# Kernel tuning notes

Hardware: AMD Instinct MI355X
Metric: run time of the kernel (lower is better)

Reference implementation:

```python
import jax, jax.numpy as jnp
import numpy as np
from jax import lax

B, S, D, T = 128, 512, 512, 64
OUT = 3


def setup_inputs() -> dict:
    key = jax.random.key(0)
    ks = jax.random.split(key, 16)
    sd = 0.05
    return {
        "e_all": jax.random.normal(ks[0], (B, S, D), jnp.float32),
        "e_last": jax.random.normal(ks[1], (1, B, D), jnp.float32),
        "target": jax.random.normal(ks[2], (B, T, OUT), jnp.float32),
        # attention params
        "Wa": jax.random.normal(ks[3], (D, D), jnp.float32) * sd,
        "ba": jnp.zeros((D,), jnp.float32),
        "Ua": jax.random.normal(ks[4], (D, D), jnp.float32) * sd,
        "bu": jnp.zeros((D,), jnp.float32),
        "Va_w": jax.random.normal(ks[5], (1, D), jnp.float32) * sd,
        "Va_b": jnp.zeros((1,), jnp.float32),
        # GRU params (PyTorch layout: [3D, in], gates order r,z,n)
        "W_ih": jax.random.normal(ks[6], (3 * D, D + OUT), jnp.float32) * sd,
        "b_ih": jnp.zeros((3 * D,), jnp.float32),
        "W_hh": jax.random.normal(ks[7], (3 * D, D), jnp.float32) * sd,
        "b_hh": jnp.zeros((3 * D,), jnp.float32),
        # output projection
        "W_out": jax.random.normal(ks[8], (OUT, D), jnp.float32) * sd,
        "b_out": jnp.zeros((OUT,), jnp.float32),
    }


def reference(e_all, e_last, target, Wa, ba, Ua, bu, Va_w, Va_b,
              W_ih, b_ih, W_hh, b_hh, W_out, b_out):
    # Precompute Ua(keys): keys are fixed across timesteps (same math as per-step).
    Uk = jnp.einsum('bsd,ed->bse', e_all, Ua) + bu        # [B,S,D]
    va = Va_w[0]                                          # [D]

    def step(h, x):
        # h: [B,D] decoder hidden; x: [B,3] decoder input (dropout is eval/identity)
        q = h @ Wa.T + ba                                  # [B,D]
        scores = jnp.einsum('bsd,d->bs', jnp.tanh(q[:, None, :] + Uk), va) + Va_b[0]
        w = jax.nn.softmax(scores, axis=-1)                # [B,S]
        ctx = jnp.einsum('bs,bsd->bd', w, e_all)           # [B,D]
        gin = jnp.concatenate([ctx, x], axis=-1)           # [B,D+3]  (attn first)
        gi = gin @ W_ih.T + b_ih                           # [B,3D]
        gh = h @ W_hh.T + b_hh                             # [B,3D]
        i_r, i_z, i_n = jnp.split(gi, 3, axis=-1)
        h_r, h_z, h_n = jnp.split(gh, 3, axis=-1)
        r = jax.nn.sigmoid(i_r + h_r)
        z = jax.nn.sigmoid(i_z + h_z)
        n = jnp.tanh(i_n + r * h_n)
        h_new = (1.0 - z) * n + z * h                      # [B,D]
        out = h_new @ W_out.T + b_out                      # [B,3]
        return h_new, (out, w)

    # teacher forcing: step 0 sees zeros, step i sees target[:, i-1]
    xs = jnp.concatenate([jnp.zeros((1, B, OUT), e_all.dtype),
                          jnp.swapaxes(target[:, :T - 1, :], 0, 1)], axis=0)  # [T,B,3]
    hT, (outs, attns) = lax.scan(step, e_last[0], xs)
    d_outputs = jnp.swapaxes(outs, 0, 1)     # [B,T,3]
    cross_attn = jnp.swapaxes(attns, 0, 1)   # [B,T,S]
    return d_outputs, hT[None], cross_attn
```

## Files before the change

kernel.cpp:

```cpp
#include <hip/hip_runtime.h>
#include <cstdint>

constexpr int BB = 128;
constexpr int SS = 512;
constexpr int DD = 512;
constexpr int TT = 64;
constexpr int OO = 3;

constexpr float C2LE = 2.8853900817779268f;

typedef __attribute__((ext_vector_type(8))) short bf16x8;
typedef __attribute__((ext_vector_type(4))) float f32x4;

__device__ __forceinline__ float tanh_fast(float x) {
  float e = __expf(2.0f * x);
  return 1.0f - 2.0f / (e + 1.0f);
}
__device__ __forceinline__ float sigmoid_fast(float x) {
  return 1.0f / (1.0f + __expf(-x));
}
__device__ __forceinline__ unsigned short f2bf(float f) {
  uint32_t u = __float_as_uint(f);
  uint32_t r = (u + 0x7FFFu + ((u >> 16) & 1u)) >> 16;
  return (unsigned short)r;
}
__device__ __forceinline__ float bf2f(unsigned short h) {
  return __uint_as_float((uint32_t)h << 16);
}
__device__ __forceinline__ float2 bfx2(uint32_t u) {
  float2 r;
  r.x = __uint_as_float(u << 16);
  r.y = __uint_as_float(u & 0xFFFF0000u);
  return r;
}
__device__ __forceinline__ float fexp2(float x) {
#if __has_builtin(__builtin_amdgcn_exp2f)
  return __builtin_amdgcn_exp2f(x);
#else
  return exp2f(x);
#endif
}
__device__ __forceinline__ float frcp(float x) {
#if __has_builtin(__builtin_amdgcn_rcpf)
  return __builtin_amdgcn_rcpf(x);
#else
  return 1.0f / x;
#endif
}

__global__ __launch_bounds__(256) void gemm_uk_mfma(
    const unsigned short* __restrict__ A, const unsigned short* __restrict__ Bw,
    const float* __restrict__ bias, unsigned short* __restrict__ Uk) {
  __shared__ unsigned short Asb[128 * 40];
  __shared__ unsigned short Bsb[128 * 40];
  const int tid = threadIdx.x;
  const int m0 = blockIdx.y * 128, n0 = blockIdx.x * 128;
  const int w = tid >> 6, l = tid & 63;
  const int wr = w >> 1, wc = w & 1;
  const int lm = l & 15, kg = l >> 4;

  f32x4 acc[4][4] = {};

  for (int kc = 0; kc < 512; kc += 32) {
    uint4 av[2], bv[2];
#pragma unroll
    for (int p = 0; p < 2; ++p) {
      int u = tid + p * 256;
      int r = u >> 2, ko = (u & 3) * 8;
      av[p] = *(const uint4*)(A + (size_t)(m0 + r) * 512 + kc + ko);
      bv[p] = *(const uint4*)(Bw + (size_t)(n0 + r) * 512 + kc + ko);
    }
    __syncthreads();
#pragma unroll
    for (int p = 0; p < 2; ++p) {
      int u = tid + p * 256;
      int r = u >> 2, ko = (u & 3) * 8;
      *(uint4*)&Asb[r * 40 + ko] = av[p];
      *(uint4*)&Bsb[r * 40 + ko] = bv[p];
    }
    __syncthreads();
    bf16x8 af[4], bfr[4];
#pragma unroll
    for (int i = 0; i < 4; ++i) {
      af[i]  = *(const bf16x8*)&Asb[(wr * 64 + i * 16 + lm) * 40 + kg * 8];
      bfr[i] = *(const bf16x8*)&Bsb[(wc * 64 + i * 16 + lm) * 40 + kg * 8];
    }
#pragma unroll
    for (int i = 0; i < 4; ++i)
#pragma unroll
      for (int j = 0; j < 4; ++j)
        acc[i][j] = __builtin_amdgcn_mfma_f32_16x16x32_bf16(af[i], bfr[j],
                                                            acc[i][j], 0, 0, 0);
  }

  const int row_base = m0 + wr * 64;
  const int col_base = n0 + wc * 64;
#pragma unroll
  for (int j = 0; j < 4; ++j) {
    const int col = col_base + j * 16 + lm;
    const float bu = bias[col];
#pragma unroll
    for (int i = 0; i < 4; ++i) {
      const int r0 = row_base + i * 16 + kg * 4;
#pragma unroll
      for (int rr = 0; rr < 4; ++rr)
        Uk[(size_t)(r0 + rr) * 512 + col] = f2bf(C2LE * (acc[i][j][rr] + bu));
    }
  }
}

__global__ __launch_bounds__(256) void conv_bf(const float* __restrict__ in,
                                               unsigned short* __restrict__ outp) {
  size_t idx = ((size_t)blockIdx.x * 256 + threadIdx.x) * 8;
  const float4* p = (const float4*)(in + idx);
  float4 a = p[0], b = p[1];
  uint4 r;
  r.x = f2bf(a.x) | ((uint32_t)f2bf(a.y) << 16);
  r.y = f2bf(a.z) | ((uint32_t)f2bf(a.w) << 16);
  r.z = f2bf(b.x) | ((uint32_t)f2bf(b.y) << 16);
  r.w = f2bf(b.z) | ((uint32_t)f2bf(b.w) << 16);
  *(uint4*)(outp + idx) = r;
}

__global__ void prep_wq2(const float* __restrict__ Wa,
                         unsigned short* __restrict__ Wq2) {
  int idx = blockIdx.x * 256 + threadIdx.x;
  Wq2[idx] = f2bf(C2LE * Wa[idx]);
}

__global__ void prep_wih3(const float* __restrict__ W_ih,
                          unsigned short* __restrict__ Wih3) {
  int idx = blockIdx.x * 256 + threadIdx.x;
  int rp = idx >> 9, k = idx & 511;
  int dgrp = rp / 48, rem = rp % 48;
  int g = rem >> 4, dl = rem & 15;
  int src = g * 512 + dgrp * 16 + dl;
  Wih3[idx] = f2bf(W_ih[(size_t)src * (DD + OO) + k]);
}

__global__ void prep_whh3(const float* __restrict__ Whh,
                          unsigned short* __restrict__ Whh3) {
  int idx = blockIdx.x * 256 + threadIdx.x;
  int rp = idx >> 9, k = idx & 511;
  int dgrp = rp / 48, rem = rp % 48;
  int g = rem >> 4, dl = rem & 15;
  int src = g * 512 + dgrp * 16 + dl;
  Whh3[idx] = f2bf(Whh[(size_t)src * DD + k]);
}

__global__ void prep_bq(const float* __restrict__ ba, float* __restrict__ bq) {
  int j = blockIdx.x * 256 + threadIdx.x;
  bq[j] = C2LE * ba[j];
}

__global__ void init_h(const float* __restrict__ e_last,
                       float* __restrict__ out_hT,
                       unsigned short* __restrict__ h2g) {
  int idx = blockIdx.x * 256 + threadIdx.x;
  int b = idx >> 9, d = idx & 511;
  float v = e_last[idx];
  out_hT[idx] = v;
  unsigned short hi = f2bf(v);
  h2g[(size_t)b * 1024 + d] = hi;
  h2g[(size_t)b * 1024 + 512 + d] = f2bf(v - bf2f(hi));
}

__global__ __launch_bounds__(1024) void qgemm_out(
    const unsigned short* __restrict__ h2g, const unsigned short* __restrict__ Wq2,
    const float* __restrict__ bq, float* __restrict__ q2g,
    const float* __restrict__ out_hT, const float* __restrict__ W_out,
    const float* __restrict__ b_out, float* __restrict__ out_d, int t) {
  const int blk = blockIdx.x, tid = threadIdx.x;
  __shared__ unsigned short As[128 * 136];
  __shared__ unsigned short Bs[32 * 136];
  if (blk < 16) {
    const int w = tid >> 6, l = tid & 63, lm = l & 15, kg = l >> 4;
    const int n0 = blk * 32;
    const int mi = w >> 1, jt = w & 1;
    f32x4 acc = {};
    for (int kc = 0; kc < 1024; kc += 128) {
#pragma unroll
      for (int p = 0; p < 2; ++p) {
        int u = tid + p * 1024;
        int r = u >> 4, ko = (u & 15) * 8;
        *(uint4*)&As[r * 136 + ko] =
            *(const uint4*)&h2g[(size_t)r * 1024 + kc + ko];
      }
      if (tid < 512) {
        int r = tid >> 4, ko = (tid & 15) * 8;
        *(uint4*)&Bs[r * 136 + ko] =
            *(const uint4*)&Wq2[(size_t)(n0 + r) * 512 + (kc & 511) + ko];
      }
      __syncthreads();
#pragma unroll
      for (int ks = 0; ks < 4; ++ks) {
        bf16x8 af = *(const bf16x8*)&As[(mi * 16 + lm) * 136 + ks * 32 + kg * 8];
        bf16x8 bf_ = *(const bf16x8*)&Bs[(jt * 16 + lm) * 136 + ks * 32 + kg * 8];
        acc = __builtin_amdgcn_mfma_f32_16x16x32_bf16(af, bf_, acc, 0, 0, 0);
      }
      __syncthreads();
    }
    const int col = n0 + jt * 16 + lm;
    const float bias = bq[col];
#pragma unroll
    for (int rr = 0; rr < 4; ++rr) {
      const int b = mi * 16 + kg * 4 + rr;
      q2g[(size_t)b * 512 + col] = acc[rr] + bias;
    }
  } else if (t > 0) {
    const int b = tid >> 3, g8 = tid & 7;
    const float* hp = out_hT + (size_t)b * DD + g8 * 64;
#pragma unroll
    for (int o = 0; o < OO; ++o) {
      const float* wrow = W_out + (size_t)o * DD + g8 * 64;
      float acc = 0.f;
#pragma unroll 8
      for (int i = 0; i < 64; ++i) acc += hp[i] * wrow[i];
      acc += __shfl_down(acc, 4, 8);
      acc += __shfl_down(acc, 2, 8);
      acc += __shfl_down(acc, 1, 8);
      if (g8 == 0) out_d[((size_t)b * TT + (t - 1)) * OO + o] = acc + b_out[o];
    }
  }
}

__global__ __launch_bounds__(256) void attn_scores(
    const unsigned short* __restrict__ Uk2, const float* __restrict__ q2g,
    const float* __restrict__ va, float* __restrict__ scores) {
  const int b = blockIdx.y;
  const int s0 = blockIdx.x * 64;
  __shared__ float4 shq[DD / 4];
  __shared__ float4 shva[DD / 4];
  const int tid = threadIdx.x;
  if (tid < DD / 4) {
    shq[tid] = ((const float4*)(q2g + (size_t)b * DD))[tid];
    shva[tid] = ((const float4*)va)[tid];
  }
  __syncthreads();
  const int g = tid >> 4, l = tid & 15;
#pragma unroll
  for (int i = 0; i < 4; ++i) {
    const int s = s0 + 16 * i + g;
    const uint4* row = (const uint4*)(Uk2 + ((size_t)b * SS + s) * DD);
    float acc = 0.f;
#pragma unroll
    for (int jj = 0; jj < 4; ++jj) {
      const int slot = l + 16 * jj;
      uint4 u = row[slot];
      float4 q0 = shq[slot * 2], q1 = shq[slot * 2 + 1];
      float4 v0 = shva[slot * 2], v1 = shva[slot * 2 + 1];
      float2 e0 = bfx2(u.x), e1 = bfx2(u.y), e2 = bfx2(u.z), e3 = bfx2(u.w);
      acc += v0.x * frcp(1.f + fexp2(q0.x + e0.x));
      acc += v0.y * frcp(1.f + fexp2(q0.y + e0.y));
      acc += v0.z * frcp(1.f + fexp2(q0.z + e1.x));
      acc += v0.w * frcp(1.f + fexp2(q0.w + e1.y));
      acc += v1.x * frcp(1.f + fexp2(q1.x + e2.x));
      acc += v1.y * frcp(1.f + fexp2(q1.y + e2.y));
      acc += v1.z * frcp(1.f + fexp2(q1.z + e3.x));
      acc += v1.w * frcp(1.f + fexp2(q1.w + e3.y));
    }
#pragma unroll
    for (int off = 8; off; off >>= 1) acc += __shfl_down(acc, off, 16);
    if (l == 0) scores[(size_t)b * SS + s] = -2.f * acc;
  }
}

__global__ __launch_bounds__(256) void attn_ctx(
    const unsigned short* __restrict__ e_bf, const float* __restrict__ scores,
    float* __restrict__ ctx, float* __restrict__ attn_out, int t) {
  const int b = blockIdx.y, dc = blockIdx.x;
  __shared__ float w[SS];
  __shared__ float red[8];
  __shared__ float part[16][132];
  const int tid = threadIdx.x;

  float v0 = scores[(size_t)b * SS + tid];
  float v1 = scores[(size_t)b * SS + 256 + tid];
  float m = fmaxf(v0, v1);
#pragma unroll
  for (int off = 32; off; off >>= 1) m = fmaxf(m, __shfl_xor(m, off));
  if ((tid & 63) == 0) red[tid >> 6] = m;
  __syncthreads();
  m = fmaxf(fmaxf(red[0], red[1]), fmaxf(red[2], red[3]));
  float e0 = __expf(v0 - m), e1 = __expf(v1 - m);
  float ss = e0 + e1;
#pragma unroll
  for (int off = 32; off; off >>= 1) ss += __shfl_xor(ss, off);
  __syncthreads();
  if ((tid & 63) == 0) red[tid >> 6] = ss;
  __syncthreads();
  const float inv = 1.f / (red[0] + red[1] + red[2] + red[3]);
  float w0 = e0 * inv, w1 = e1 * inv;
  w[tid] = w0;
  w[tid + 256] = w1;
  if (dc == 0) {
    float* ao = attn_out + ((size_t)b * TT + t) * SS;
    ao[tid] = w0;
    ao[tid + 256] = w1;
  }
  __syncthreads();

  {
    const int sl = tid & 15, sg = tid >> 4;
    const unsigned short* eb = e_bf + (size_t)b * SS * DD + dc * 128 + sl * 8;
    float a0 = 0.f, a1 = 0.f, a2 = 0.f, a3 = 0.f;
    float a4 = 0.f, a5 = 0.f, a6 = 0.f, a7 = 0.f;
    for (int s = sg * 32; s < sg * 32 + 32; ++s) {
      uint4 u = *(const uint4*)(eb + (size_t)s * DD);
      float ws = w[s];
      float2 p0 = bfx2(u.x), p1 = bfx2(u.y), p2 = bfx2(u.z), p3 = bfx2(u.w);
      a0 += ws * p0.x; a1 += ws * p0.y;
      a2 += ws * p1.x; a3 += ws * p1.y;
      a4 += ws * p2.x; a5 += ws * p2.y;
      a6 += ws * p3.x; a7 += ws * p3.y;
    }
    float* pr = &part[sg][sl * 8];
    pr[0] = a0; pr[1] = a1; pr[2] = a2; pr[3] = a3;
    pr[4] = a4; pr[5] = a5; pr[6] = a6; pr[7] = a7;
  }
  __syncthreads();
  if (tid < 128) {
    const int sl = tid >> 3, c = tid & 7;
    float r = 0.f;
#pragma unroll
    for (int sg = 0; sg < 16; ++sg) r += part[sg][sl * 8 + c];
    ctx[(size_t)b * DD + dc * 128 + sl * 8 + c] = r;
  }
}

__global__ __launch_bounds__(1024) void gru_fused(
    const float* __restrict__ ctx, unsigned short* __restrict__ h2g,
    const unsigned short* __restrict__ Wih3, const unsigned short* __restrict__ Whh3,
    float* __restrict__ out_hT, const float* __restrict__ target,
    const float* __restrict__ W_ih, const float* __restrict__ b_ih,
    const float* __restrict__ b_hh, int t) {
  const int blk = blockIdx.x, tid = threadIdx.x;
  const int w = tid >> 6, l = tid & 63, lm = l & 15, kg = l >> 4;
  const int mh = blk >> 5, dgrp = blk & 31;

  __shared__ unsigned short Ach[32 * 72];
  __shared__ unsigned short Acl[32 * 72];
  __shared__ unsigned short Ahh[32 * 72];
  __shared__ unsigned short Ahl[32 * 72];
  __shared__ unsigned short Bih[48 * 72];
  __shared__ unsigned short Bhh[48 * 72];

  float wx[3][3], pbih[3], pbhh[3];
  if (w < 2) {
    const int d = dgrp * 16 + lm;
#pragma unroll
    for (int g = 0; g < 3; ++g) {
      const float* wp = W_ih + (size_t)(g * 512 + d) * (DD + OO) + DD;
      wx[g][0] = wp[0]; wx[g][1] = wp[1]; wx[g][2] = wp[2];
      pbih[g] = b_ih[g * 512 + d];
      pbhh[g] = b_hh[g * 512 + d];
    }
  }

  f32x4 aci[3] = {};
  f32x4 agh[3] = {};
  for (int kc = 0; kc < 512; kc += 64) {
    if (tid < 256) {
      int r = tid >> 3, ko = (tid & 7) * 8;
      int b = mh * 32 + r;
      const float* p0 = &ctx[(size_t)b * 512 + kc + ko];
      float4 a0 = *(const float4*)p0, a1 = *(const float4*)(p0 + 4);
      float v[8] = {a0.x, a0.y, a0.z, a0.w, a1.x, a1.y, a1.z, a1.w};
      uint32_t H[4], L[4];
#pragma unroll
      for (int i = 0; i < 4; ++i) {
        unsigned short h0 = f2bf(v[2 * i]), h1 = f2bf(v[2 * i + 1]);
        unsigned short l0_ = f2bf(v[2 * i] - bf2f(h0));
        unsigned short l1_ = f2bf(v[2 * i + 1] - bf2f(h1));
        H[i] = (uint32_t)h0 | ((uint32_t)h1 << 16);
        L[i] = (uint32_t)l0_ | ((uint32_t)l1_ << 16);
      }
      *(uint4*)&Ach[r * 72 + ko] = *(uint4*)H;
      *(uint4*)&Acl[r * 72 + ko] = *(uint4*)L;
    } else if (tid < 512) {
      int u = tid - 256;
      int r = u >> 3, ko = (u & 7) * 8;
      int b = mh * 32 + r;
      *(uint4*)&Ahh[r * 72 + ko] =
          *(const uint4*)&h2g[(size_t)b * 1024 + kc + ko];
      *(uint4*)&Ahl[r * 72 + ko] =
          *(const uint4*)&h2g[(size_t)b * 1024 + 512 + kc + ko];
    } else if (tid < 896) {
      int u = tid - 512;
      int r = u >> 3, ko = (u & 7) * 8;
      *(uint4*)&Bih[r * 72 + ko] =
          *(const uint4*)&Wih3[(size_t)(dgrp * 48 + r) * 512 + kc + ko];
      *(uint4*)&Bhh[r * 72 + ko] =
          *(const uint4*)&Whh3[(size_t)(dgrp * 48 + r) * 512 + kc + ko];
    }
    __syncthreads();
    if (w < 2) {
#pragma unroll
      for (int ks = 0; ks < 2; ++ks) {
        const int ao = (w * 16 + lm) * 72 + ks * 32 + kg * 8;
        bf16x8 ach_ = *(const bf16x8*)&Ach[ao];
        bf16x8 acl_ = *(const bf16x8*)&Acl[ao];
        bf16x8 ahh_ = *(const bf16x8*)&Ahh[ao];
        bf16x8 ahl_ = *(const bf16x8*)&Ahl[ao];
#pragma unroll
        for (int g = 0; g < 3; ++g) {
          const int bo = (g * 16 + lm) * 72 + ks * 32 + kg * 8;
          bf16x8 bi = *(const bf16x8*)&Bih[bo];
          bf16x8 bh = *(const bf16x8*)&Bhh[bo];
          aci[g] = __builtin_amdgcn_mfma_f32_16x16x32_bf16(ach_, bi, aci[g], 0, 0, 0);
          aci[g] = __builtin_amdgcn_mfma_f32_16x16x32_bf16(acl_, bi, aci[g], 0, 0, 0);
          agh[g] = __builtin_amdgcn_mfma_f32_16x16x32_bf16(ahh_, bh, agh[g], 0, 0, 0);
          agh[g] = __builtin_amdgcn_mfma_f32_16x16x32_bf16(ahl_, bh, agh[g], 0, 0, 0);
        }
      }
    }
    __syncthreads();
  }

  if (w < 2) {
    const int d = dgrp * 16 + lm;
#pragma unroll
    for (int rr = 0; rr < 4; ++rr) {
      const int b = mh * 32 + w * 16 + kg * 4 + rr;
      float x0 = 0.f, x1 = 0.f, x2 = 0.f;
      if (t > 0) {
        const float* xp = target + ((size_t)b * TT + (t - 1)) * OO;
        x0 = xp[0]; x1 = xp[1]; x2 = xp[2];
      }
      float ir = aci[0][rr] + pbih[0] + x0 * wx[0][0] + x1 * wx[0][1] + x2 * wx[0][2];
      float iz = aci[1][rr] + pbih[1] + x0 * wx[1][0] + x1 * wx[1][1] + x2 * wx[1][2];
      float in_ = aci[2][rr] + pbih[2] + x0 * wx[2][0] + x1 * wx[2][1] + x2 * wx[2][2];
      float hr = agh[0][rr] + pbhh[0];
      float hz = agh[1][rr] + pbhh[1];
      float hn = agh[2][rr] + pbhh[2];
      float r_ = sigmoid_fast(ir + hr);
      float z_ = sigmoid_fast(iz + hz);
      float n_ = tanh_fast(in_ + r_ * hn);
      float hold = out_hT[(size_t)b * DD + d];
      float hnew = (1.f - z_) * n_ + z_ * hold;
      out_hT[(size_t)b * DD + d] = hnew;
      unsigned short hhi = f2bf(hnew);
      h2g[(size_t)b * 1024 + d] = hhi;
      h2g[(size_t)b * 1024 + 512 + d] = f2bf(hnew - bf2f(hhi));
    }
  }
}

extern "C" void kernel_launch(void* const* d_in, const int* in_sizes, int n_in,
                              void* d_out, int out_size, void* d_ws, size_t ws_size,
                              hipStream_t stream) {
  const float* e_all  = (const float*)d_in[0];
  const float* e_last = (const float*)d_in[1];
  const float* target = (const float*)d_in[2];
  const float* Wa     = (const float*)d_in[3];
  const float* ba     = (const float*)d_in[4];
  const float* Ua     = (const float*)d_in[5];
  const float* bu     = (const float*)d_in[6];
  const float* Va_w   = (const float*)d_in[7];
  const float* W_ih   = (const float*)d_in[9];
  const float* b_ih   = (const float*)d_in[10];
  const float* W_hh   = (const float*)d_in[11];
  const float* b_hh   = (const float*)d_in[12];
  const float* W_out  = (const float*)d_in[13];
  const float* b_out  = (const float*)d_in[14];

  float* out      = (float*)d_out;
  float* out_d    = out;
  float* out_hT   = out + (size_t)BB * TT * OO;
  float* out_attn = out_hT + (size_t)BB * DD;

  char* wsB = (char*)d_ws;
  unsigned short* Uk2   = (unsigned short*)wsB;
  unsigned short* e_bfp = (unsigned short*)(wsB + 67108864);
  unsigned short* Wq2   = (unsigned short*)(wsB + 134217728);
  unsigned short* Wih3  = (unsigned short*)(wsB + 134742016);
  unsigned short* Whh3  = (unsigned short*)(wsB + 136314880);
  float* bq             = (float*)(wsB + 137887744);
  unsigned short* h2    = (unsigned short*)(wsB + 137889792);
  float* q2g            = (float*)(wsB + 138151936);
  float* ctx            = (float*)(wsB + 138414080);
  float* scores         = (float*)(wsB + 138676224);
  unsigned short* Ua_bf = (unsigned short*)(wsB + 137889792);

  prep_wq2<<<(DD * DD) / 256, 256, 0, stream>>>(Wa, Wq2);
  prep_wih3<<<(1536 * 512) / 256, 256, 0, stream>>>(W_ih, Wih3);
  prep_whh3<<<(1536 * 512) / 256, 256, 0, stream>>>(W_hh, Whh3);
  prep_bq<<<2, 256, 0, stream>>>(ba, bq);
  conv_bf<<<(BB * SS * DD) / (8 * 256), 256, 0, stream>>>(e_all, e_bfp);
  conv_bf<<<(DD * DD) / (8 * 256), 256, 0, stream>>>(Ua, Ua_bf);
  gemm_uk_mfma<<<dim3(DD / 128, (BB * SS) / 128), 256, 0, stream>>>(
      e_bfp, Ua_bf, bu, Uk2);
  init_h<<<(BB * DD) / 256, 256, 0, stream>>>(e_last, out_hT, h2);

  for (int t = 0; t < TT; ++t) {
    qgemm_out<<<17, 1024, 0, stream>>>(h2, Wq2, bq, q2g, out_hT, W_out, b_out,
                                       out_d, t);
    attn_scores<<<dim3(SS / 64, BB), 256, 0, stream>>>(Uk2, q2g, Va_w, scores);
    attn_ctx<<<dim3(4, BB), 256, 0, stream>>>(e_bfp, scores, ctx, out_attn, t);
    gru_fused<<<128, 1024, 0, stream>>>(ctx, h2, Wih3, Whh3, out_hT, target,
                                        W_ih, b_ih, b_hh, t);
  }
  qgemm_out<<<17, 1024, 0, stream>>>(h2, Wq2, bq, q2g, out_hT, W_out, b_out,
                                     out_d, TT);
}
```

Measured before the change: 5.481 ms.

## Fuse query GEMM, scores, softmax and context into one per-batch-half kernel

Replaces the per-step q-GEMM, score and context kernels with one attn_fused kernel. Each block covers one batch row and half the sequence: it computes q from fp32 h against a transposed bf16 Wa, then the scores, a local softmax and a partial context. The two halves are merged flash-style inside gru_fused using the per-half max and sum, and that kernel also writes the normalized attention weights. This cuts per-step launches from four to two and removes global round-trips for q and the scores. In exchange, every block re-reads the whole 512x512 Wq matrix, and only 256 blocks run during the bandwidth-heavy phase.

```diff
diff --git a/kernel.cpp b/kernel.cpp
--- a/kernel.cpp
+++ b/kernel.cpp
@@ -122,10 +122,11 @@
   *(uint4*)(outp + idx) = r;
 }
 
-__global__ void prep_wq2(const float* __restrict__ Wa,
-                         unsigned short* __restrict__ Wq2) {
+__global__ void prep_wq2t(const float* __restrict__ Wa,
+                          unsigned short* __restrict__ Wq2t) {
   int idx = blockIdx.x * 256 + threadIdx.x;
-  Wq2[idx] = f2bf(C2LE * Wa[idx]);
+  int k = idx >> 9, j = idx & 511;
+  Wq2t[idx] = f2bf(C2LE * Wa[(size_t)j * DD + k]);
 }
 
 __global__ void prep_wih3(const float* __restrict__ W_ih,
@@ -165,90 +166,67 @@
   h2g[(size_t)b * 1024 + 512 + d] = f2bf(v - bf2f(hi));
 }
 
-__global__ __launch_bounds__(1024) void qgemm_out(
-    const unsigned short* __restrict__ h2g, const unsigned short* __restrict__ Wq2,
-    const float* __restrict__ bq, float* __restrict__ q2g,
-    const float* __restrict__ out_hT, const float* __restrict__ W_out,
-    const float* __restrict__ b_out, float* __restrict__ out_d, int t) {
+__global__ __launch_bounds__(512) void attn_fused(
+    const unsigned short* __restrict__ Uk2, const unsigned short* __restrict__ e_bf,
+    const unsigned short* __restrict__ Wq2t, const float* __restrict__ bq,
+    const float* __restrict__ va, const float* __restrict__ out_hT,
+    float* __restrict__ ctxp, float* __restrict__ stats, float* __restrict__ uw,
+    const float* __restrict__ W_out, const float* __restrict__ b_out,
+    float* __restrict__ out_d, int t) {
   const int blk = blockIdx.x, tid = threadIdx.x;
-  __shared__ unsigned short As[128 * 136];
-  __shared__ unsigned short Bs[32 * 136];
-  if (blk < 16) {
-    const int w = tid >> 6, l = tid & 63, lm = l & 15, kg = l >> 4;
-    const int n0 = blk * 32;
-    const int mi = w >> 1, jt = w & 1;
-    f32x4 acc = {};
-    for (int kc = 0; kc < 1024; kc += 128) {
-#pragma unroll
-      for (int p = 0; p < 2; ++p) {
-        int u = tid + p * 1024;
-        int r = u >> 4, ko = (u & 15) * 8;
-        *(uint4*)&As[r * 136 + ko] =
-            *(const uint4*)&h2g[(size_t)r * 1024 + kc + ko];
+  if (blk == 256) {
+    if (t > 0) {
+      const int b = tid >> 2, g4 = tid & 3;
+      const float* hp = out_hT + (size_t)b * DD + g4 * 128;
+#pragma unroll
+      for (int o = 0; o < OO; ++o) {
+        const float* wrow = W_out + (size_t)o * DD + g4 * 128;
+        float acc = 0.f;
+#pragma unroll 8
+        for (int i = 0; i < 128; ++i) acc += hp[i] * wrow[i];
+        acc += __shfl_down(acc, 2, 4);
+        acc += __shfl_down(acc, 1, 4);
+        if (g4 == 0) out_d[((size_t)b * TT + (t - 1)) * OO + o] = acc + b_out[o];
       }
-      if (tid < 512) {
-        int r = tid >> 4, ko = (tid & 15) * 8;
-        *(uint4*)&Bs[r * 136 + ko] =
-            *(const uint4*)&Wq2[(size_t)(n0 + r) * 512 + (kc & 511) + ko];
-      }
-      __syncthreads();
-#pragma unroll
-      for (int ks = 0; ks < 4; ++ks) {
-        bf16x8 af = *(const bf16x8*)&As[(mi * 16 + lm) * 136 + ks * 32 + kg * 8];
-        bf16x8 bf_ = *(const bf16x8*)&Bs[(jt * 16 + lm) * 136 + ks * 32 + kg * 8];
-        acc = __builtin_amdgcn_mfma_f32_16x16x32_bf16(af, bf_, acc, 0, 0, 0);
-      }
-      __syncthreads();
-    }
-    const int col = n0 + jt * 16 + lm;
-    const float bias = bq[col];
-#pragma unroll
-    for (int rr = 0; rr < 4; ++rr) {
-      const int b = mi * 16 + kg * 4 + rr;
-      q2g[(size_t)b * 512 + col] = acc[rr] + bias;
-    }
-  } else if (t > 0) {
-    const int b = tid >> 3, g8 = tid & 7;
-    const float* hp = out_hT + (size_t)b * DD + g8 * 64;
-#pragma unroll
-    for (int o = 0; o < OO; ++o) {
-      const float* wrow = W_out + (size_t)o * DD + g8 * 64;
-      float acc = 0.f;
+    }
+    return;
+  }
+  const int b = blk >> 1, shalf = blk & 1;
+
+  __shared__ float h_s[512];
+  __shared__ float qv_s[4 * 132];
+  __shared__ float va_s[4 * 132];
+  __shared__ float u_s[256];
+  __shared__ float red_s[16];
+  __shared__ float part[8 * 520];
+
+  h_s[tid] = out_hT[(size_t)b * DD + tid];
+  va_s[(tid >> 7) * 132 + (tid & 127)] = va[tid];
+  __syncthreads();
+
+  {
+    float acc = 0.f;
+    const unsigned short* wp = Wq2t + tid;
 #pragma unroll 8
-      for (int i = 0; i < 64; ++i) acc += hp[i] * wrow[i];
-      acc += __shfl_down(acc, 4, 8);
-      acc += __shfl_down(acc, 2, 8);
-      acc += __shfl_down(acc, 1, 8);
-      if (g8 == 0) out_d[((size_t)b * TT + (t - 1)) * OO + o] = acc + b_out[o];
-    }
-  }
-}
-
-__global__ __launch_bounds__(256) void attn_scores(
-    const unsigned short* __restrict__ Uk2, const float* __restrict__ q2g,
-    const float* __restrict__ va, float* __restrict__ scores) {
-  const int b = blockIdx.y;
-  const int s0 = blockIdx.x * 64;
-  __shared__ float4 shq[DD / 4];
-  __shared__ float4 shva[DD / 4];
-  const int tid = threadIdx.x;
-  if (tid < DD / 4) {
-    shq[tid] = ((const float4*)(q2g + (size_t)b * DD))[tid];
-    shva[tid] = ((const float4*)va)[tid];
+    for (int k = 0; k < 512; ++k) acc += h_s[k] * bf2f(wp[(size_t)k * 512]);
+    acc += bq[tid];
+    qv_s[(tid >> 7) * 132 + (tid & 127)] = acc;
   }
   __syncthreads();
-  const int g = tid >> 4, l = tid & 15;
-#pragma unroll
-  for (int i = 0; i < 4; ++i) {
-    const int s = s0 + 16 * i + g;
-    const uint4* row = (const uint4*)(Uk2 + ((size_t)b * SS + s) * DD);
+
+  {
+    const int sl = tid >> 1, hf = tid & 1;
+    const uint4* up =
+        (const uint4*)(Uk2 + ((size_t)b * SS + shalf * 256 + sl) * DD + hf * 256);
     float acc = 0.f;
-#pragma unroll
-    for (int jj = 0; jj < 4; ++jj) {
-      const int slot = l + 16 * jj;
-      uint4 u = row[slot];
-      float4 q0 = shq[slot * 2], q1 = shq[slot * 2 + 1];
-      float4 v0 = shva[slot * 2], v1 = shva[slot * 2 + 1];
+#pragma unroll 4
+    for (int j = 0; j < 32; ++j) {
+      uint4 u = up[j];
+      const int qq = (hf << 1) + (j >> 4), jj = j & 15;
+      const float* qb = &qv_s[qq * 132 + jj * 8];
+      const float* vb = &va_s[qq * 132 + jj * 8];
+      float4 q0 = *(const float4*)&qb[0], q1 = *(const float4*)&qb[4];
+      float4 v0 = *(const float4*)&vb[0], v1 = *(const float4*)&vb[4];
       float2 e0 = bfx2(u.x), e1 = bfx2(u.y), e2 = bfx2(u.z), e3 = bfx2(u.w);
       acc += v0.x * frcp(1.f + fexp2(q0.x + e0.x));
       acc += v0.y * frcp(1.f + fexp2(q0.y + e0.y));
@@ -259,81 +237,74 @@
       acc += v1.z * frcp(1.f + fexp2(q1.z + e3.x));
       acc += v1.w * frcp(1.f + fexp2(q1.w + e3.y));
     }
-#pragma unroll
-    for (int off = 8; off; off >>= 1) acc += __shfl_down(acc, off, 16);
-    if (l == 0) scores[(size_t)b * SS + s] = -2.f * acc;
-  }
-}
-
-__global__ __launch_bounds__(256) void attn_ctx(
-    const unsigned short* __restrict__ e_bf, const float* __restrict__ scores,
-    float* __restrict__ ctx, float* __restrict__ attn_out, int t) {
-  const int b = blockIdx.y, dc = blockIdx.x;
-  __shared__ float w[SS];
-  __shared__ float red[8];
-  __shared__ float part[16][132];
-  const int tid = threadIdx.x;
-
-  float v0 = scores[(size_t)b * SS + tid];
-  float v1 = scores[(size_t)b * SS + 256 + tid];
-  float m = fmaxf(v0, v1);
-#pragma unroll
-  for (int off = 32; off; off >>= 1) m = fmaxf(m, __shfl_xor(m, off));
-  if ((tid & 63) == 0) red[tid >> 6] = m;
+    acc += __shfl_xor(acc, 1);
+    if (hf == 0) u_s[sl] = -2.f * acc;
+  }
   __syncthreads();
-  m = fmaxf(fmaxf(red[0], red[1]), fmaxf(red[2], red[3]));
-  float e0 = __expf(v0 - m), e1 = __expf(v1 - m);
-  float ss = e0 + e1;
-#pragma unroll
-  for (int off = 32; off; off >>= 1) ss += __shfl_xor(ss, off);
+
+  {
+    const int w4 = tid >> 6;
+    float y = (tid < 256) ? u_s[tid] : -3.0e38f;
+    float m = y;
+#pragma unroll
+    for (int off = 32; off; off >>= 1) m = fmaxf(m, __shfl_xor(m, off));
+    if (w4 < 4 && (tid & 63) == 0) red_s[w4] = m;
+    __syncthreads();
+    const float gm = fmaxf(fmaxf(red_s[0], red_s[1]), fmaxf(red_s[2], red_s[3]));
+    float e = (tid < 256) ? __expf(y - gm) : 0.f;
+    float sm = e;
+#pragma unroll
+    for (int off = 32; off; off >>= 1) sm += __shfl_xor(sm, off);
+    if (w4 < 4 && (tid & 63) == 0) red_s[8 + w4] = sm;
+    __syncthreads();
+    if (tid < 256) {
+      u_s[tid] = e;
+      uw[(size_t)b * SS + shalf * 256 + tid] = e;
+    }
+    if (tid == 0) {
+      stats[b * 4 + shalf * 2] = gm;
+      stats[b * 4 + shalf * 2 + 1] = red_s[8] + red_s[9] + red_s[10] + red_s[11];
+    }
+  }
   __syncthreads();
-  if ((tid & 63) == 0) red[tid >> 6] = ss;
-  __syncthreads();
-  const float inv = 1.f / (red[0] + red[1] + red[2] + red[3]);
-  float w0 = e0 * inv, w1 = e1 * inv;
-  w[tid] = w0;
-  w[tid + 256] = w1;
-  if (dc == 0) {
-    float* ao = attn_out + ((size_t)b * TT + t) * SS;
-    ao[tid] = w0;
-    ao[tid + 256] = w1;
-  }
-  __syncthreads();
 
   {
-    const int sl = tid & 15, sg = tid >> 4;
-    const unsigned short* eb = e_bf + (size_t)b * SS * DD + dc * 128 + sl * 8;
+    const int dsl = tid & 63, sg = tid >> 6;
+    const unsigned short* eb =
+        e_bf + ((size_t)b * SS + shalf * 256 + sg * 32) * DD + dsl * 8;
     float a0 = 0.f, a1 = 0.f, a2 = 0.f, a3 = 0.f;
     float a4 = 0.f, a5 = 0.f, a6 = 0.f, a7 = 0.f;
-    for (int s = sg * 32; s < sg * 32 + 32; ++s) {
-      uint4 u = *(const uint4*)(eb + (size_t)s * DD);
-      float ws = w[s];
+#pragma unroll 4
+    for (int si = 0; si < 32; ++si) {
+      uint4 u = *(const uint4*)(eb + (size_t)si * DD);
+      float ws = u_s[sg * 32 + si];
       float2 p0 = bfx2(u.x), p1 = bfx2(u.y), p2 = bfx2(u.z), p3 = bfx2(u.w);
       a0 += ws * p0.x; a1 += ws * p0.y;
       a2 += ws * p1.x; a3 += ws * p1.y;
       a4 += ws * p2.x; a5 += ws * p2.y;
       a6 += ws * p3.x; a7 += ws * p3.y;
     }
-    float* pr = &part[sg][sl * 8];
-    pr[0] = a0; pr[1] = a1; pr[2] = a2; pr[3] = a3;
-    pr[4] = a4; pr[5] = a5; pr[6] = a6; pr[7] = a7;
+    float* pr = &part[sg * 520 + dsl * 8];
+    float4 lo = {a0, a1, a2, a3}, hi = {a4, a5, a6, a7};
+    *(float4*)&pr[0] = lo;
+    *(float4*)&pr[4] = hi;
   }
   __syncthreads();
-  if (tid < 128) {
-    const int sl = tid >> 3, c = tid & 7;
+  {
     float r = 0.f;
 #pragma unroll
-    for (int sg = 0; sg < 16; ++sg) r += part[sg][sl * 8 + c];
-    ctx[(size_t)b * DD + dc * 128 + sl * 8 + c] = r;
+    for (int sg = 0; sg < 8; ++sg) r += part[sg * 520 + tid];
+    ctxp[((size_t)b * 2 + shalf) * 512 + tid] = r;
   }
 }
 
 __global__ __launch_bounds__(1024) void gru_fused(
-    const float* __restrict__ ctx, unsigned short* __restrict__ h2g,
+    const float* __restrict__ ctxp, unsigned short* __restrict__ h2g,
     const unsigned short* __restrict__ Wih3, const unsigned short* __restrict__ Whh3,
     float* __restrict__ out_hT, const float* __restrict__ target,
     const float* __restrict__ W_ih, const float* __restrict__ b_ih,
-    const float* __restrict__ b_hh, int t) {
+    const float* __restrict__ b_hh, const float* __restrict__ stats,
+    const float* __restrict__ uw, float* __restrict__ out_attn, int t) {
   const int blk = blockIdx.x, tid = threadIdx.x;
   const int w = tid >> 6, l = tid & 63, lm = l & 15, kg = l >> 4;
   const int mh = blk >> 5, dgrp = blk & 31;
@@ -344,6 +315,17 @@
   __shared__ unsigned short Ahl[32 * 72];
   __shared__ unsigned short Bih[48 * 72];
   __shared__ unsigned short Bhh[48 * 72];
+  __shared__ float als[64];
+
+  if (tid < 32) {
+    const int bb = mh * 32 + tid;
+    float m0 = stats[bb * 4], l0 = stats[bb * 4 + 1];
+    float m1 = stats[bb * 4 + 2], l1 = stats[bb * 4 + 3];
+    float M = fmaxf(m0, m1);
+    float iZ = 1.f / (l0 * __expf(m0 - M) + l1 * __expf(m1 - M));
+    als[tid * 2] = __expf(m0 - M) * iZ;
+    als[tid * 2 + 1] = __expf(m1 - M) * iZ;
+  }
 
   float wx[3][3], pbih[3], pbhh[3];
   if (w < 2) {
@@ -355,6 +337,17 @@
       pbih[g] = b_ih[g * 512 + d];
       pbhh[g] = b_hh[g * 512 + d];
     }
+  }
+  __syncthreads();
+
+  if (tid >= 896) {
+    const int b_att = mh * 32 + dgrp;
+    const float a0 = als[dgrp * 2], a1 = als[dgrp * 2 + 1];
+    const float* up = uw + (size_t)b_att * SS;
+    float* ao = out_attn + ((size_t)b_att * TT + t) * SS;
+    const int i0 = (tid - 896) * 4;
+#pragma unroll
+    for (int i = i0; i < i0 + 4; ++i) ao[i] = up[i] * ((i < 256) ? a0 : a1);
   }
 
   f32x4 aci[3] = {};
@@ -363,9 +356,15 @@
     if (tid < 256) {
       int r = tid >> 3, ko = (tid & 7) * 8;
       int b = mh * 32 + r;
-      const float* p0 = &ctx[(size_t)b * 512 + kc + ko];
-      float4 a0 = *(const float4*)p0, a1 = *(const float4*)(p0 + 4);
-      float v[8] = {a0.x, a0.y, a0.z, a0.w, a1.x, a1.y, a1.z, a1.w};
+      const float a0 = als[r * 2], a1 = als[r * 2 + 1];
+      const float* p0 = &ctxp[((size_t)b * 2) * 512 + kc + ko];
+      const float* p1 = &ctxp[((size_t)b * 2 + 1) * 512 + kc + ko];
+      float4 c0a = *(const float4*)p0, c0b = *(const float4*)(p0 + 4);
+      float4 c1a = *(const float4*)p1, c1b = *(const float4*)(p1 + 4);
+      float v[8] = {a0 * c0a.x + a1 * c1a.x, a0 * c0a.y + a1 * c1a.y,
+                    a0 * c0a.z + a1 * c1a.z, a0 * c0a.w + a1 * c1a.w,
+                    a0 * c0b.x + a1 * c1b.x, a0 * c0b.y + a1 * c1b.y,
+                    a0 * c0b.z + a1 * c1b.z, a0 * c0b.w + a1 * c1b.w};
       uint32_t H[4], L[4];
 #pragma unroll
       for (int i = 0; i < 4; ++i) {
@@ -446,6 +445,24 @@
   }
 }
 
+__global__ __launch_bounds__(512) void outproj_tail(
+    const float* __restrict__ out_hT, const float* __restrict__ W_out,
+    const float* __restrict__ b_out, float* __restrict__ out_d) {
+  const int tid = threadIdx.x;
+  const int b = tid >> 2, g4 = tid & 3;
+  const float* hp = out_hT + (size_t)b * DD + g4 * 128;
+#pragma unroll
+  for (int o = 0; o < OO; ++o) {
+    const float* wrow = W_out + (size_t)o * DD + g4 * 128;
+    float acc = 0.f;
+#pragma unroll 8
+    for (int i = 0; i < 128; ++i) acc += hp[i] * wrow[i];
+    acc += __shfl_down(acc, 2, 4);
+    acc += __shfl_down(acc, 1, 4);
+    if (g4 == 0) out_d[((size_t)b * TT + (TT - 1)) * OO + o] = acc + b_out[o];
+  }
+}
+
 extern "C" void kernel_launch(void* const* d_in, const int* in_sizes, int n_in,
                               void* d_out, int out_size, void* d_ws, size_t ws_size,
                               hipStream_t stream) {
@@ -472,17 +489,17 @@
   char* wsB = (char*)d_ws;
   unsigned short* Uk2   = (unsigned short*)wsB;
   unsigned short* e_bfp = (unsigned short*)(wsB + 67108864);
-  unsigned short* Wq2   = (unsigned short*)(wsB + 134217728);
+  unsigned short* Wq2t  = (unsigned short*)(wsB + 134217728);
   unsigned short* Wih3  = (unsigned short*)(wsB + 134742016);
   unsigned short* Whh3  = (unsigned short*)(wsB + 136314880);
   float* bq             = (float*)(wsB + 137887744);
   unsigned short* h2    = (unsigned short*)(wsB + 137889792);
-  float* q2g            = (float*)(wsB + 138151936);
-  float* ctx            = (float*)(wsB + 138414080);
-  float* scores         = (float*)(wsB + 138676224);
+  float* uw             = (float*)(wsB + 138151936);
+  float* ctxp           = (float*)(wsB + 138414080);
+  float* stats          = (float*)(wsB + 138938368);
   unsigned short* Ua_bf = (unsigned short*)(wsB + 137889792);
 
-  prep_wq2<<<(DD * DD) / 256, 256, 0, stream>>>(Wa, Wq2);
+  prep_wq2t<<<(DD * DD) / 256, 256, 0, stream>>>(Wa, Wq2t);
   prep_wih3<<<(1536 * 512) / 256, 256, 0, stream>>>(W_ih, Wih3);
   prep_whh3<<<(1536 * 512) / 256, 256, 0, stream>>>(W_hh, Whh3);
   prep_bq<<<2, 256, 0, stream>>>(ba, bq);
@@ -493,13 +510,10 @@
   init_h<<<(BB * DD) / 256, 256, 0, stream>>>(e_last, out_hT, h2);
 
   for (int t = 0; t < TT; ++t) {
-    qgemm_out<<<17, 1024, 0, stream>>>(h2, Wq2, bq, q2g, out_hT, W_out, b_out,
-                                       out_d, t);
-    attn_scores<<<dim3(SS / 64, BB), 256, 0, stream>>>(Uk2, q2g, Va_w, scores);
-    attn_ctx<<<dim3(4, BB), 256, 0, stream>>>(e_bfp, scores, ctx, out_attn, t);
-    gru_fused<<<128, 1024, 0, stream>>>(ctx, h2, Wih3, Whh3, out_hT, target,
-                                        W_ih, b_ih, b_hh, t);
-  }
-  qgemm_out<<<17, 1024, 0, stream>>>(h2, Wq2, bq, q2g, out_hT, W_out, b_out,
-                                     out_d, TT);
-}
+    attn_fused<<<257, 512, 0, stream>>>(Uk2, e_bfp, Wq2t, bq, Va_w, out_hT,
+                                        ctxp, stats, uw, W_out, b_out, out_d, t);
+    gru_fused<<<128, 1024, 0, stream>>>(ctxp, h2, Wih3, Whh3, out_hT, target,
+                                        W_ih, b_ih, b_hh, stats, uw, out_attn, t);
+  }
+  outproj_tail<<<1, 512, 0, stream>>>(out_hT, W_out, b_out, out_d);
+}
```

Result: slower. 6.039 ms (+10.2%).
